# Performance work log

Measured on AMD Instinct MI355X. Metric: run time of the kernel, lower is better.

## Reference

```python
import jax, jax.numpy as jnp
import numpy as np

DN = ('NCHW', 'OIHW', 'NCHW')

def _conv(x, w, b, pad):
    y = jax.lax.conv_general_dilated(x, w, (1, 1), pad, dimension_numbers=DN)
    return y + b[None, :, None, None]

def setup_inputs() -> dict:
    key = jax.random.key(0)
    ks = jax.random.split(key, 8)
    B, C, H, W = 8, 256, 64, 64
    C8 = C // 8
    return {
        'x': jax.random.normal(ks[0], (B, C, H, W), jnp.float32),
        'wq': jax.random.normal(ks[1], (C8, C, 1, 3), jnp.float32) * 0.02,
        'bq': jax.random.normal(ks[2], (C8,), jnp.float32) * 0.02,
        'wk': jax.random.normal(ks[3], (C8, C, 3, 1), jnp.float32) * 0.02,
        'bk': jax.random.normal(ks[4], (C8,), jnp.float32) * 0.02,
        'wv': jax.random.normal(ks[5], (C, C, 1, 1), jnp.float32) * 0.02,
        'bv': jax.random.normal(ks[6], (C,), jnp.float32) * 0.02,
        'gamma': jax.random.normal(ks[7], (1,), jnp.float32),
    }

def reference(x, wq, bq, wk, bk, wv, bv, gamma):
    B, C, H, W = x.shape
    N = H * W
    # q: (1,3) kernel, pad (0,1); k: (3,1) kernel, pad (1,0); v: 1x1
    q = _conv(x, wq, bq, [(0, 0), (1, 1)]).reshape(B, -1, N)  # B, C/8, N
    k = _conv(x, wk, bk, [(1, 1), (0, 0)]).reshape(B, -1, N)  # B, C/8, N
    v = _conv(x, wv, bv, [(0, 0), (0, 0)]).reshape(B, C, N)   # B, C, N
    affinity = jnp.einsum('bci,bcj->bij', q, k)               # B, N, N
    affinity = jax.nn.softmax(affinity, axis=-1)
    # weights = v @ affinity^T  ->  (B, C, N)
    weights = jnp.einsum('bcj,bij->bci', v, affinity).reshape(B, C, H, W)
    return gamma[0] * weights + x
```

## Files before the change

kernel.cpp:

```cpp
#include <hip/hip_runtime.h>
#include <math.h>

#define BB 8
#define CCH 256
#define C8 32
#define NN 4096
#define LOG2E 1.44269504f

typedef unsigned short us;
typedef __attribute__((ext_vector_type(8))) short bf16x8;
typedef __attribute__((ext_vector_type(4))) float f32x4;
typedef __attribute__((ext_vector_type(16))) float f32x16;

static __device__ __forceinline__ us f2bf(float f) {
  union { float f; unsigned u; } v; v.f = f;
  unsigned r = v.u + 0x7fffu + ((v.u >> 16) & 1u);
  return (us)(r >> 16);
}

__global__ __launch_bounds__(256) void prep_kernel(
    const float* __restrict__ x, const float* __restrict__ wq,
    const float* __restrict__ wk, const float* __restrict__ wv,
    us* __restrict__ xT, us* __restrict__ wqc, us* __restrict__ wkc,
    us* __restrict__ wvb) {
  __shared__ __align__(16) us lt[64 * 68];
  int bid = blockIdx.x;
  int tid = threadIdx.x;
  if (bid < 2048) {
    int b = bid >> 8, cb = (bid >> 6) & 3, nb = bid & 63;
    const float* xb = x + (((size_t)(b * 256 + cb * 64)) << 12);
    int nl = tid & 63, ch = tid >> 6;
#pragma unroll
    for (int p = 0; p < 16; p++) {
      int c = p * 4 + ch;
      lt[nl * 68 + c] = f2bf(xb[((size_t)c << 12) + (nb * 64 + nl)]);
    }
    __syncthreads();
    us* xTb = xT + (((size_t)b << 12) + nb * 64) * 256 + cb * 64;
    int cw = tid & 7, nr0 = tid >> 3;
#pragma unroll
    for (int p2 = 0; p2 < 2; p2++) {
      int nr = p2 * 32 + nr0;
      uint2 lo = *(const uint2*)&lt[nr * 68 + cw * 8];
      uint2 hi = *(const uint2*)&lt[nr * 68 + cw * 8 + 4];
      *(uint4*)&xTb[(size_t)nr * 256 + cw * 8] = make_uint4(lo.x, lo.y, hi.x, hi.y);
    }
  } else {
    int idx = (bid - 2048) * 256 + tid;
    if (idx < 24576) {
      int oc = idx / 768, r = idx % 768, t = r >> 8, ic = r & 255;
      wqc[idx] = f2bf(wq[(oc * 256 + ic) * 3 + t] * LOG2E);
    } else if (idx < 49152) {
      int j = idx - 24576;
      int oc = j / 768, r = j % 768, t = r >> 8, ic = r & 255;
      wkc[j] = f2bf(wk[(oc * 256 + ic) * 3 + t]);
    } else if (idx < 114688) {
      int j = idx - 49152;
      wvb[j] = f2bf(wv[j]);
    }
  }
}

__global__ __launch_bounds__(256) void conv_kernel(
    const us* __restrict__ xT, const us* __restrict__ wqc,
    const us* __restrict__ wkc, const float* __restrict__ bq,
    const float* __restrict__ bk, const us* __restrict__ wvb,
    const float* __restrict__ bv, us* __restrict__ qT, us* __restrict__ kT,
    us* __restrict__ vblk) {
  int tid = threadIdx.x, lane = tid & 63, w = tid >> 6;
  int l15 = lane & 15, quad = lane >> 4;
  if (blockIdx.x < 512) {
    int bid = blockIdx.x;
    int b = bid & 7, rt = bid >> 3;
    int n0 = rt * 64, y = rt;
    bool isq = (w < 2);
    int m0 = (w & 1) * 16;
    const us* wc = isq ? wqc : wkc;
    const us* xTb = xT + (((size_t)b << 12) * 256);
    f32x4 acc[4];
#pragma unroll
    for (int nt = 0; nt < 4; nt++) acc[nt] = (f32x4){0.f, 0.f, 0.f, 0.f};
#pragma unroll
    for (int t = 0; t < 3; t++) {
      bool killT = (!isq) && ((t == 0 && y == 0) || (t == 2 && y == 63));
      if (!killT) {
        int dn = isq ? (t - 1) : (t - 1) * 64;
#pragma unroll
        for (int k8 = 0; k8 < 8; k8++) {
          int kloc = t * 256 + k8 * 32 + quad * 8;
          bf16x8 af = *(const bf16x8*)(wc + (size_t)(m0 + l15) * 768 + kloc);
          int ic = k8 * 32 + quad * 8;
#pragma unroll
          for (int nt = 0; nt < 4; nt++) {
            int nl = nt * 16 + l15;
            int ns = n0 + nl + dn;
            ns = ns < 0 ? 0 : (ns > 4095 ? 4095 : ns);
            bf16x8 bf = *(const bf16x8*)(xTb + (size_t)ns * 256 + ic);
            if (isq && ((t == 0 && nl == 0) || (t == 2 && nl == 63)))
              bf = (bf16x8){0, 0, 0, 0, 0, 0, 0, 0};
            acc[nt] = __builtin_amdgcn_mfma_f32_16x16x32_bf16(af, bf, acc[nt], 0, 0, 0);
          }
        }
      }
    }
    const float* bias = isq ? bq : bk;
    float bsc = isq ? LOG2E : 1.0f;
    us* outp = (isq ? qT : kT) + (((size_t)b << 12) * 32);
    float b0 = bias[m0 + quad * 4 + 0] * bsc;
    float b1 = bias[m0 + quad * 4 + 1] * bsc;
    float b2 = bias[m0 + quad * 4 + 2] * bsc;
    float b3 = bias[m0 + quad * 4 + 3] * bsc;
#pragma unroll
    for (int nt = 0; nt < 4; nt++) {
      int n = n0 + nt * 16 + l15;
      unsigned lo = (unsigned)f2bf(acc[nt][0] + b0) | ((unsigned)f2bf(acc[nt][1] + b1) << 16);
      unsigned hi = (unsigned)f2bf(acc[nt][2] + b2) | ((unsigned)f2bf(acc[nt][3] + b3) << 16);
      *(uint2*)(outp + (size_t)n * 32 + m0 + quad * 4) = make_uint2(lo, hi);
    }
  } else {
    int bid = blockIdx.x - 512;
    int b = bid & 7, nt0 = bid >> 3;
    int n0 = nt0 * 64;
    const us* xTb = xT + (((size_t)b << 12) * 256);
    f32x4 acc[4][4];
#pragma unroll
    for (int ct = 0; ct < 4; ct++)
#pragma unroll
      for (int nt = 0; nt < 4; nt++) acc[ct][nt] = (f32x4){0.f, 0.f, 0.f, 0.f};
#pragma unroll
    for (int kk = 0; kk < 8; kk++) {
      bf16x8 bfr[4];
#pragma unroll
      for (int nt = 0; nt < 4; nt++)
        bfr[nt] = *(const bf16x8*)(xTb + (size_t)(n0 + nt * 16 + l15) * 256 + kk * 32 + quad * 8);
#pragma unroll
      for (int ct = 0; ct < 4; ct++) {
        bf16x8 af = *(const bf16x8*)(wvb + (size_t)(w * 64 + ct * 16 + l15) * 256 + kk * 32 + quad * 8);
#pragma unroll
        for (int nt = 0; nt < 4; nt++)
          acc[ct][nt] = __builtin_amdgcn_mfma_f32_16x16x32_bf16(af, bfr[nt], acc[ct][nt], 0, 0, 0);
      }
    }
    us* vb = vblk + ((size_t)b << 20);
#pragma unroll
    for (int ct = 0; ct < 4; ct++) {
#pragma unroll
      for (int r = 0; r < 4; r++) {
        int oc = w * 64 + ct * 16 + quad * 4 + r;
        float bvv = bv[oc];
#pragma unroll
        for (int nt = 0; nt < 4; nt++) {
          vb[((size_t)((n0 >> 4) + nt) * 256 + oc) * 16 + l15] = f2bf(acc[ct][nt][r] + bvv);
        }
      }
    }
  }
}

__global__ __launch_bounds__(512, 4) void attn_kernel(
    const float* __restrict__ x, const us* __restrict__ qT,
    const us* __restrict__ kT, const us* __restrict__ vblk,
    const float* __restrict__ gamma_p, float* __restrict__ out) {
  __shared__ __align__(16) us pb[2][64 * 72];
  __shared__ float lpart[2][64];

  int tid = threadIdx.x, lane = tid & 63, w = tid >> 6;
  int l15 = lane & 15, quad = lane >> 4;
  int l31 = lane & 31, h32 = lane >> 5;
  int tw = w & 3, jh = w >> 2;

  int bid = blockIdx.x;
  int b = bid & 7, i0 = (bid >> 3) * 64;

  const us* qTb = qT + (((size_t)b << 12) * 32);
  const us* kTb = kT + (((size_t)b << 12) * 32);
  const us* vbb = vblk + ((size_t)b << 20);

  bf16x8 qf = *(const bf16x8*)(qTb + (size_t)(i0 + tw * 16 + l15) * 32 + quad * 8);

  const us* kbase = kTb + (size_t)(jh * 32 + l15) * 32 + quad * 8;
  const us* vbase = vbb + (size_t)(w * 32 + l31) * 16 + h32 * 8;
  int pwi = (tw * 16 + l15) * 72 + jh * 32 + quad * 4;
  int pri = l31 * 72 + h32 * 8;

  float lr = 0.f;
  f32x4 s0, s1;
  f32x16 o0, o1;
#pragma unroll
  for (int rg = 0; rg < 16; rg++) { o0[rg] = 0.f; o1[rg] = 0.f; }

  bf16x8 kS0a, kS0b, kS1a, kS1b;
  bf16x8 v0_0, v0_1, v0_2, v0_3;
  bf16x8 v1_0, v1_1, v1_2, v1_3;
  bf16x8 v2_0, v2_1, v2_2, v2_3;
  bf16x8 v3_0, v3_1, v3_2, v3_3;

#define PRE(JT, KN0, KN1, VN0, VN1, VN2, VN3)                                  \
  do {                                                                         \
    int jn = (JT) & 63;                                                        \
    const us* kp = kbase + (size_t)jn * 2048;                                  \
    const us* vp = vbase + (size_t)jn * 16384;                                 \
    KN0 = *(const bf16x8*)(kp);                                                \
    KN1 = *(const bf16x8*)(kp + 512);                                          \
    VN0 = *(const bf16x8*)(vp);                                                \
    VN1 = *(const bf16x8*)(vp + 4096);                                         \
    VN2 = *(const bf16x8*)(vp + 8192);                                         \
    VN3 = *(const bf16x8*)(vp + 12288);                                        \
  } while (0)

#define QKM(KC0, KC1)                                                          \
  do {                                                                         \
    s0 = __builtin_amdgcn_mfma_f32_16x16x32_bf16(KC0, qf, (f32x4){0.f, 0.f, 0.f, 0.f}, 0, 0, 0); \
    s1 = __builtin_amdgcn_mfma_f32_16x16x32_bf16(KC1, qf, (f32x4){0.f, 0.f, 0.f, 0.f}, 0, 0, 0); \
  } while (0)

#define PVM(BUFR, VP0, VP1, VP2, VP3)                                          \
  do {                                                                         \
    const us* pr = (const us*)pb + (BUFR) * (64 * 72) + pri;                   \
    __builtin_amdgcn_s_setprio(1);                                             \
    bf16x8 pf0, pf1;                                                           \
    pf0 = *(const bf16x8*)(pr + 0);                                            \
    pf1 = *(const bf16x8*)(pr + 32 * 72 + 0);                                  \
    o0 = __builtin_amdgcn_mfma_f32_32x32x16_bf16(VP0, pf0, o0, 0, 0, 0);       \
    o1 = __builtin_amdgcn_mfma_f32_32x32x16_bf16(VP0, pf1, o1, 0, 0, 0);       \
    pf0 = *(const bf16x8*)(pr + 16);                                           \
    pf1 = *(const bf16x8*)(pr + 32 * 72 + 16);                                 \
    o0 = __builtin_amdgcn_mfma_f32_32x32x16_bf16(VP1, pf0, o0, 0, 0, 0);       \
    o1 = __builtin_amdgcn_mfma_f32_32x32x16_bf16(VP1, pf1, o1, 0, 0, 0);       \
    pf0 = *(const bf16x8*)(pr + 32);                                           \
    pf1 = *(const bf16x8*)(pr + 32 * 72 + 32);                                 \
    o0 = __builtin_amdgcn_mfma_f32_32x32x16_bf16(VP2, pf0, o0, 0, 0, 0);       \
    o1 = __builtin_amdgcn_mfma_f32_32x32x16_bf16(VP2, pf1, o1, 0, 0, 0);       \
    pf0 = *(const bf16x8*)(pr + 48);                                           \
    pf1 = *(const bf16x8*)(pr + 32 * 72 + 48);                                 \
    o0 = __builtin_amdgcn_mfma_f32_32x32x16_bf16(VP3, pf0, o0, 0, 0, 0);       \
    o1 = __builtin_amdgcn_mfma_f32_32x32x16_bf16(VP3, pf1, o1, 0, 0, 0);       \
    __builtin_amdgcn_s_setprio(0);                                             \
  } while (0)

#define SMW(BUFW)                                                              \
  do {                                                                         \
    us* pw = (us*)pb + (BUFW) * (64 * 72) + pwi;                               \
    {                                                                          \
      float p0 = __builtin_amdgcn_exp2f(s0[0]);                                \
      float p1 = __builtin_amdgcn_exp2f(s0[1]);                                \
      float p2 = __builtin_amdgcn_exp2f(s0[2]);                                \
      float p3 = __builtin_amdgcn_exp2f(s0[3]);                                \
      lr += (p0 + p1) + (p2 + p3);                                             \
      unsigned e0, e1;                                                         \
      asm("v_cvt_pk_bf16_f32 %0, %1, %2" : "=v"(e0) : "v"(p0), "v"(p1));       \
      asm("v_cvt_pk_bf16_f32 %0, %1, %2" : "=v"(e1) : "v"(p2), "v"(p3));       \
      *(uint2*)pw = make_uint2(e0, e1);                                        \
    }                                                                          \
    {                                                                          \
      float p0 = __builtin_amdgcn_exp2f(s1[0]);                                \
      float p1 = __builtin_amdgcn_exp2f(s1[1]);                                \
      float p2 = __builtin_amdgcn_exp2f(s1[2]);                                \
      float p3 = __builtin_amdgcn_exp2f(s1[3]);                                \
      lr += (p0 + p1) + (p2 + p3);                                             \
      unsigned e0, e1;                                                         \
      asm("v_cvt_pk_bf16_f32 %0, %1, %2" : "=v"(e0) : "v"(p0), "v"(p1));       \
      asm("v_cvt_pk_bf16_f32 %0, %1, %2" : "=v"(e1) : "v"(p2), "v"(p3));       \
      *(uint2*)(pw + 16) = make_uint2(e0, e1);                                 \
    }                                                                          \
  } while (0)

#define BAR                                                                    \
  do {                                                                         \
    asm volatile("s_waitcnt lgkmcnt(0)" ::: "memory");                         \
    __builtin_amdgcn_s_barrier();                                              \
    __builtin_amdgcn_sched_barrier(0);                                         \
  } while (0)

  PRE(0, kS0a, kS0b, v0_0, v0_1, v0_2, v0_3);
  PRE(1, kS1a, kS1b, v1_0, v1_1, v1_2, v1_3);
  QKM(kS0a, kS0b);
  SMW(0);
  BAR;
  PRE(2, kS0a, kS0b, v2_0, v2_1, v2_2, v2_3);
  QKM(kS1a, kS1b);
  PVM(0, v0_0, v0_1, v0_2, v0_3);
  SMW(1);
  BAR;
  PRE(3, kS1a, kS1b, v3_0, v3_1, v3_2, v3_3);
  QKM(kS0a, kS0b);
  PVM(1, v1_0, v1_1, v1_2, v1_3);
  SMW(0);
  BAR;
  PRE(4, kS0a, kS0b, v0_0, v0_1, v0_2, v0_3);
  QKM(kS1a, kS1b);
  PVM(0, v2_0, v2_1, v2_2, v2_3);
  SMW(1);
  BAR;

  for (int n4 = 1; n4 < 16; n4++) {
    int n = n4 * 4;
    PRE(n + 1, kS1a, kS1b, v1_0, v1_1, v1_2, v1_3);
    QKM(kS0a, kS0b);
    PVM(1, v3_0, v3_1, v3_2, v3_3);
    SMW(0);
    BAR;
    PRE(n + 2, kS0a, kS0b, v2_0, v2_1, v2_2, v2_3);
    QKM(kS1a, kS1b);
    PVM(0, v0_0, v0_1, v0_2, v0_3);
    SMW(1);
    BAR;
    PRE(n + 3, kS1a, kS1b, v3_0, v3_1, v3_2, v3_3);
    QKM(kS0a, kS0b);
    PVM(1, v1_0, v1_1, v1_2, v1_3);
    SMW(0);
    BAR;
    PRE(n + 4, kS0a, kS0b, v0_0, v0_1, v0_2, v0_3);
    QKM(kS1a, kS1b);
    PVM(0, v2_0, v2_1, v2_2, v2_3);
    SMW(1);
    BAR;
  }
  PVM(1, v3_0, v3_1, v3_2, v3_3);

#undef PRE
#undef QKM
#undef PVM
#undef SMW
#undef BAR

  float lt = lr;
  lt += __shfl_xor(lt, 16);
  lt += __shfl_xor(lt, 32);
  if (quad == 0) lpart[jh][tw * 16 + l15] = lt;
  __syncthreads();
  float g = gamma_p[0];
  const float* xb = x + ((size_t)b << 20);
  float* ob = out + ((size_t)b << 20);
  float gl[2];
#pragma unroll
  for (int it = 0; it < 2; it++) {
    int i = it * 32 + l31;
    gl[it] = g / (lpart[0][i] + lpart[1][i]);
  }
#pragma unroll
  for (int it = 0; it < 2; it++) {
    int i = i0 + it * 32 + l31;
    const f32x16& o = (it == 0) ? o0 : o1;
#pragma unroll
    for (int rg = 0; rg < 16; rg++) {
      int c = w * 32 + ((rg & 3) + 8 * (rg >> 2) + 4 * h32);
      size_t idx = ((size_t)c << 12) + i;
      ob[idx] = o[rg] * gl[it] + xb[idx];
    }
  }
}

extern "C" void kernel_launch(void* const* d_in, const int* in_sizes, int n_in,
                              void* d_out, int out_size, void* d_ws, size_t ws_size,
                              hipStream_t stream) {
  const float* x = (const float*)d_in[0];
  const float* wq = (const float*)d_in[1];
  const float* bq = (const float*)d_in[2];
  const float* wk = (const float*)d_in[3];
  const float* bk = (const float*)d_in[4];
  const float* wv = (const float*)d_in[5];
  const float* bv = (const float*)d_in[6];
  const float* gamma = (const float*)d_in[7];
  float* out = (float*)d_out;

  us* xT = (us*)d_ws;
  us* qT = xT + (size_t)8388608;
  us* kT = qT + (size_t)1048576;
  us* vblk = kT + (size_t)1048576;
  us* wqc = vblk + (size_t)8388608;
  us* wkc = wqc + (size_t)24576;
  us* wvb = wkc + (size_t)24576;

  prep_kernel<<<2496, 256, 0, stream>>>(x, wq, wk, wv, xT, wqc, wkc, wvb);
  conv_kernel<<<1024, 256, 0, stream>>>(xT, wqc, wkc, bq, bk, wvb, bv, qT, kT, vblk);
  attn_kernel<<<512, 512, 0, stream>>>(x, qT, kT, vblk, gamma, out);
}
```

Baseline: 228.1 us.

## Fuse x transpose into conv kernel via swizzled LDS staging

Removes the separate prep pass that wrote a bf16 transposed copy of x to global memory. The conv kernel now loads a 256-row tile of x (with 64-row halos) directly from fp32, converts it to bf16 into an XOR-swizzled 128KB LDS buffer, and computes q, k and v projections from LDS. This cuts a global round trip and a launch, at the cost of large LDS use, 1024-thread blocks with one block per CU, and redundant halo loading.

```diff
diff --git a/kernel.cpp b/kernel.cpp
--- a/kernel.cpp
+++ b/kernel.cpp
@@ -1,10 +1,6 @@
 #include <hip/hip_runtime.h>
 #include <math.h>
 
-#define BB 8
-#define CCH 256
-#define C8 32
-#define NN 4096
 #define LOG2E 1.44269504f
 
 typedef unsigned short us;
@@ -18,87 +14,86 @@
   return (us)(r >> 16);
 }
 
-__global__ __launch_bounds__(256) void prep_kernel(
-    const float* __restrict__ x, const float* __restrict__ wq,
-    const float* __restrict__ wk, const float* __restrict__ wv,
-    us* __restrict__ xT, us* __restrict__ wqc, us* __restrict__ wkc,
+__global__ __launch_bounds__(256) void wrep_kernel(
+    const float* __restrict__ wq, const float* __restrict__ wk,
+    const float* __restrict__ wv, us* __restrict__ wqc, us* __restrict__ wkc,
     us* __restrict__ wvb) {
-  __shared__ __align__(16) us lt[64 * 68];
-  int bid = blockIdx.x;
-  int tid = threadIdx.x;
-  if (bid < 2048) {
-    int b = bid >> 8, cb = (bid >> 6) & 3, nb = bid & 63;
-    const float* xb = x + (((size_t)(b * 256 + cb * 64)) << 12);
-    int nl = tid & 63, ch = tid >> 6;
-#pragma unroll
-    for (int p = 0; p < 16; p++) {
-      int c = p * 4 + ch;
-      lt[nl * 68 + c] = f2bf(xb[((size_t)c << 12) + (nb * 64 + nl)]);
-    }
-    __syncthreads();
-    us* xTb = xT + (((size_t)b << 12) + nb * 64) * 256 + cb * 64;
-    int cw = tid & 7, nr0 = tid >> 3;
-#pragma unroll
-    for (int p2 = 0; p2 < 2; p2++) {
-      int nr = p2 * 32 + nr0;
-      uint2 lo = *(const uint2*)&lt[nr * 68 + cw * 8];
-      uint2 hi = *(const uint2*)&lt[nr * 68 + cw * 8 + 4];
-      *(uint4*)&xTb[(size_t)nr * 256 + cw * 8] = make_uint4(lo.x, lo.y, hi.x, hi.y);
-    }
-  } else {
-    int idx = (bid - 2048) * 256 + tid;
-    if (idx < 24576) {
-      int oc = idx / 768, r = idx % 768, t = r >> 8, ic = r & 255;
-      wqc[idx] = f2bf(wq[(oc * 256 + ic) * 3 + t] * LOG2E);
-    } else if (idx < 49152) {
-      int j = idx - 24576;
-      int oc = j / 768, r = j % 768, t = r >> 8, ic = r & 255;
-      wkc[j] = f2bf(wk[(oc * 256 + ic) * 3 + t]);
-    } else if (idx < 114688) {
-      int j = idx - 49152;
-      wvb[j] = f2bf(wv[j]);
-    }
-  }
-}
-
-__global__ __launch_bounds__(256) void conv_kernel(
-    const us* __restrict__ xT, const us* __restrict__ wqc,
+  int idx = blockIdx.x * 256 + threadIdx.x;
+  if (idx < 24576) {
+    int oc = idx / 768, r = idx % 768, t = r >> 8, ic = r & 255;
+    wqc[idx] = f2bf(wq[(oc * 256 + ic) * 3 + t] * LOG2E);
+  } else if (idx < 49152) {
+    int j = idx - 24576;
+    int oc = j / 768, r = j % 768, t = r >> 8, ic = r & 255;
+    wkc[j] = f2bf(wk[(oc * 256 + ic) * 3 + t]);
+  } else if (idx < 114688) {
+    int j = idx - 49152;
+    wvb[j] = f2bf(wv[j]);
+  }
+}
+
+__global__ __launch_bounds__(1024) void fconv_kernel(
+    const float* __restrict__ x, const us* __restrict__ wqc,
     const us* __restrict__ wkc, const float* __restrict__ bq,
     const float* __restrict__ bk, const us* __restrict__ wvb,
     const float* __restrict__ bv, us* __restrict__ qT, us* __restrict__ kT,
     us* __restrict__ vblk) {
+  __shared__ __align__(16) us xs[256 * 256];
+
   int tid = threadIdx.x, lane = tid & 63, w = tid >> 6;
   int l15 = lane & 15, quad = lane >> 4;
-  if (blockIdx.x < 512) {
-    int bid = blockIdx.x;
-    int b = bid & 7, rt = bid >> 3;
-    int n0 = rt * 64, y = rt;
-    bool isq = (w < 2);
-    int m0 = (w & 1) * 16;
+  int bid = blockIdx.x;
+  int b = bid >> 5, yt = bid & 31;
+  int no0 = yt * 128;
+  const float* xb = x + ((size_t)b << 20);
+
+#pragma unroll
+  for (int i = 0; i < 8; i++) {
+    int c0 = (w * 8 + i) * 2;
+    const float* xc0 = xb + ((size_t)c0 << 12);
+#pragma unroll
+    for (int rb = 0; rb < 4; rb++) {
+      int rr = rb * 64 + lane;
+      int gn = no0 - 64 + rr;
+      bool valid = (unsigned)gn < 4096u;
+      float a0 = valid ? xc0[gn] : 0.f;
+      float a1 = valid ? xc0[4096 + gn] : 0.f;
+      unsigned u;
+      asm("v_cvt_pk_bf16_f32 %0, %1, %2" : "=v"(u) : "v"(a0), "v"(a1));
+      int chunk = (c0 >> 3) ^ (rr & 31);
+      *(unsigned*)&xs[rr * 256 + chunk * 8 + (c0 & 7)] = u;
+    }
+  }
+  __syncthreads();
+
+  if (w < 8) {
+    bool isq = (w < 4);
+    int qw = isq ? w : (w - 4);
     const us* wc = isq ? wqc : wkc;
-    const us* xTb = xT + (((size_t)b << 12) * 256);
-    f32x4 acc[4];
-#pragma unroll
-    for (int nt = 0; nt < 4; nt++) acc[nt] = (f32x4){0.f, 0.f, 0.f, 0.f};
+    f32x4 acc00 = (f32x4){0.f, 0.f, 0.f, 0.f}, acc01 = acc00;
+    f32x4 acc10 = acc00, acc11 = acc00;
 #pragma unroll
     for (int t = 0; t < 3; t++) {
-      bool killT = (!isq) && ((t == 0 && y == 0) || (t == 2 && y == 63));
-      if (!killT) {
-        int dn = isq ? (t - 1) : (t - 1) * 64;
-#pragma unroll
-        for (int k8 = 0; k8 < 8; k8++) {
-          int kloc = t * 256 + k8 * 32 + quad * 8;
-          bf16x8 af = *(const bf16x8*)(wc + (size_t)(m0 + l15) * 768 + kloc);
-          int ic = k8 * 32 + quad * 8;
-#pragma unroll
-          for (int nt = 0; nt < 4; nt++) {
-            int nl = nt * 16 + l15;
-            int ns = n0 + nl + dn;
-            ns = ns < 0 ? 0 : (ns > 4095 ? 4095 : ns);
-            bf16x8 bf = *(const bf16x8*)(xTb + (size_t)ns * 256 + ic);
-            if (isq && ((t == 0 && nl == 0) || (t == 2 && nl == 63)))
-              bf = (bf16x8){0, 0, 0, 0, 0, 0, 0, 0};
-            acc[nt] = __builtin_amdgcn_mfma_f32_16x16x32_bf16(af, bf, acc[nt], 0, 0, 0);
+      int dn = isq ? (t - 1) : (t - 1) * 64;
+#pragma unroll
+      for (int k8 = 0; k8 < 8; k8++) {
+        int kloc = t * 256 + k8 * 32 + quad * 8;
+        bf16x8 af0 = *(const bf16x8*)(wc + (size_t)l15 * 768 + kloc);
+        bf16x8 af1 = *(const bf16x8*)(wc + (size_t)(16 + l15) * 768 + kloc);
+        int cb3 = (k8 * 32 + quad * 8) >> 3;
+#pragma unroll
+        for (int j = 0; j < 2; j++) {
+          int ntl = (qw * 2 + j) * 16 + l15;
+          int rr = 64 + ntl + dn;
+          bf16x8 bf = *(const bf16x8*)&xs[rr * 256 + ((cb3 ^ (rr & 31)) << 3)];
+          if (isq && ((t == 0 && (ntl & 63) == 0) || (t == 2 && (ntl & 63) == 63)))
+            bf = (bf16x8){0, 0, 0, 0, 0, 0, 0, 0};
+          if (j == 0) {
+            acc00 = __builtin_amdgcn_mfma_f32_16x16x32_bf16(af0, bf, acc00, 0, 0, 0);
+            acc10 = __builtin_amdgcn_mfma_f32_16x16x32_bf16(af1, bf, acc10, 0, 0, 0);
+          } else {
+            acc01 = __builtin_amdgcn_mfma_f32_16x16x32_bf16(af0, bf, acc01, 0, 0, 0);
+            acc11 = __builtin_amdgcn_mfma_f32_16x16x32_bf16(af1, bf, acc11, 0, 0, 0);
           }
         }
       }
@@ -106,52 +101,45 @@
     const float* bias = isq ? bq : bk;
     float bsc = isq ? LOG2E : 1.0f;
     us* outp = (isq ? qT : kT) + (((size_t)b << 12) * 32);
-    float b0 = bias[m0 + quad * 4 + 0] * bsc;
-    float b1 = bias[m0 + quad * 4 + 1] * bsc;
-    float b2 = bias[m0 + quad * 4 + 2] * bsc;
-    float b3 = bias[m0 + quad * 4 + 3] * bsc;
-#pragma unroll
-    for (int nt = 0; nt < 4; nt++) {
-      int n = n0 + nt * 16 + l15;
-      unsigned lo = (unsigned)f2bf(acc[nt][0] + b0) | ((unsigned)f2bf(acc[nt][1] + b1) << 16);
-      unsigned hi = (unsigned)f2bf(acc[nt][2] + b2) | ((unsigned)f2bf(acc[nt][3] + b3) << 16);
-      *(uint2*)(outp + (size_t)n * 32 + m0 + quad * 4) = make_uint2(lo, hi);
+#pragma unroll
+    for (int mo = 0; mo < 2; mo++) {
+      float b0 = bias[mo * 16 + quad * 4 + 0] * bsc;
+      float b1 = bias[mo * 16 + quad * 4 + 1] * bsc;
+      float b2 = bias[mo * 16 + quad * 4 + 2] * bsc;
+      float b3 = bias[mo * 16 + quad * 4 + 3] * bsc;
+#pragma unroll
+      for (int j = 0; j < 2; j++) {
+        f32x4 a = (mo == 0) ? (j == 0 ? acc00 : acc01) : (j == 0 ? acc10 : acc11);
+        int n = no0 + (qw * 2 + j) * 16 + l15;
+        unsigned lo = (unsigned)f2bf(a[0] + b0) | ((unsigned)f2bf(a[1] + b1) << 16);
+        unsigned hi = (unsigned)f2bf(a[2] + b2) | ((unsigned)f2bf(a[3] + b3) << 16);
+        *(uint2*)(outp + (size_t)n * 32 + mo * 16 + quad * 4) = make_uint2(lo, hi);
+      }
     }
   } else {
-    int bid = blockIdx.x - 512;
-    int b = bid & 7, nt0 = bid >> 3;
-    int n0 = nt0 * 64;
-    const us* xTb = xT + (((size_t)b << 12) * 256);
-    f32x4 acc[4][4];
-#pragma unroll
-    for (int ct = 0; ct < 4; ct++)
-#pragma unroll
-      for (int nt = 0; nt < 4; nt++) acc[ct][nt] = (f32x4){0.f, 0.f, 0.f, 0.f};
+    int nt = w - 8;
+    int rr = 64 + nt * 16 + l15;
+    f32x4 acc[16];
+#pragma unroll
+    for (int ot = 0; ot < 16; ot++) acc[ot] = (f32x4){0.f, 0.f, 0.f, 0.f};
 #pragma unroll
     for (int kk = 0; kk < 8; kk++) {
-      bf16x8 bfr[4];
-#pragma unroll
-      for (int nt = 0; nt < 4; nt++)
-        bfr[nt] = *(const bf16x8*)(xTb + (size_t)(n0 + nt * 16 + l15) * 256 + kk * 32 + quad * 8);
-#pragma unroll
-      for (int ct = 0; ct < 4; ct++) {
-        bf16x8 af = *(const bf16x8*)(wvb + (size_t)(w * 64 + ct * 16 + l15) * 256 + kk * 32 + quad * 8);
-#pragma unroll
-        for (int nt = 0; nt < 4; nt++)
-          acc[ct][nt] = __builtin_amdgcn_mfma_f32_16x16x32_bf16(af, bfr[nt], acc[ct][nt], 0, 0, 0);
+      int cb3 = (kk * 32 + quad * 8) >> 3;
+      bf16x8 bfr = *(const bf16x8*)&xs[rr * 256 + ((cb3 ^ (rr & 31)) << 3)];
+#pragma unroll
+      for (int ot = 0; ot < 16; ot++) {
+        bf16x8 af = *(const bf16x8*)(wvb + (size_t)(ot * 16 + l15) * 256 + kk * 32 + quad * 8);
+        acc[ot] = __builtin_amdgcn_mfma_f32_16x16x32_bf16(af, bfr, acc[ot], 0, 0, 0);
       }
     }
     us* vb = vblk + ((size_t)b << 20);
-#pragma unroll
-    for (int ct = 0; ct < 4; ct++) {
+    int n16 = yt * 8 + nt;
+#pragma unroll
+    for (int ot = 0; ot < 16; ot++) {
 #pragma unroll
       for (int r = 0; r < 4; r++) {
-        int oc = w * 64 + ct * 16 + quad * 4 + r;
-        float bvv = bv[oc];
-#pragma unroll
-        for (int nt = 0; nt < 4; nt++) {
-          vb[((size_t)((n0 >> 4) + nt) * 256 + oc) * 16 + l15] = f2bf(acc[ct][nt][r] + bvv);
-        }
+        int oc = ot * 16 + quad * 4 + r;
+        vb[((size_t)n16 * 256 + oc) * 16 + l15] = f2bf(acc[ot][r] + bv[oc]);
       }
     }
   }
@@ -364,15 +352,14 @@
   const float* gamma = (const float*)d_in[7];
   float* out = (float*)d_out;
 
-  us* xT = (us*)d_ws;
-  us* qT = xT + (size_t)8388608;
+  us* qT = (us*)d_ws;
   us* kT = qT + (size_t)1048576;
   us* vblk = kT + (size_t)1048576;
   us* wqc = vblk + (size_t)8388608;
   us* wkc = wqc + (size_t)24576;
   us* wvb = wkc + (size_t)24576;
 
-  prep_kernel<<<2496, 256, 0, stream>>>(x, wq, wk, wv, xT, wqc, wkc, wvb);
-  conv_kernel<<<1024, 256, 0, stream>>>(xT, wqc, wkc, bq, bk, wvb, bv, qT, kT, vblk);
+  wrep_kernel<<<448, 256, 0, stream>>>(wq, wk, wv, wqc, wkc, wvb);
+  fconv_kernel<<<256, 1024, 0, stream>>>(x, wqc, wkc, bq, bk, wvb, bv, qT, kT, vblk);
   attn_kernel<<<512, 512, 0, stream>>>(x, qT, kT, vblk, gamma, out);
 }
```

Result: slower. 239.2 us (+4.9%).

## Fuse prep, conv and attention into one cooperative persistent kernel

Applied to the files above, without the earlier changes.

Merges the three kernels into a single cooperative launch of 512 blocks of 512 threads. Grid-wide syncs separate the transpose/weight-cast, conv and attention phases, and a fallback path launches the same kernel three times with a phase mask. This removes two kernel launch gaps and tail drains, but the early phases now run on fewer, larger blocks, and the grid syncs add their own cost.

```diff
diff --git a/kernel.cpp b/kernel.cpp
--- a/kernel.cpp
+++ b/kernel.cpp
@@ -1,11 +1,10 @@
 #include <hip/hip_runtime.h>
+#include <hip/hip_cooperative_groups.h>
 #include <math.h>
 
-#define BB 8
-#define CCH 256
-#define C8 32
-#define NN 4096
 #define LOG2E 1.44269504f
+
+namespace cg = cooperative_groups;
 
 typedef unsigned short us;
 typedef __attribute__((ext_vector_type(8))) short bf16x8;
@@ -18,182 +17,175 @@
   return (us)(r >> 16);
 }
 
-__global__ __launch_bounds__(256) void prep_kernel(
+__global__ __launch_bounds__(512, 4) void mega_kernel(
     const float* __restrict__ x, const float* __restrict__ wq,
     const float* __restrict__ wk, const float* __restrict__ wv,
-    us* __restrict__ xT, us* __restrict__ wqc, us* __restrict__ wkc,
-    us* __restrict__ wvb) {
-  __shared__ __align__(16) us lt[64 * 68];
-  int bid = blockIdx.x;
-  int tid = threadIdx.x;
-  if (bid < 2048) {
-    int b = bid >> 8, cb = (bid >> 6) & 3, nb = bid & 63;
-    const float* xb = x + (((size_t)(b * 256 + cb * 64)) << 12);
-    int nl = tid & 63, ch = tid >> 6;
-#pragma unroll
-    for (int p = 0; p < 16; p++) {
-      int c = p * 4 + ch;
-      lt[nl * 68 + c] = f2bf(xb[((size_t)c << 12) + (nb * 64 + nl)]);
-    }
-    __syncthreads();
-    us* xTb = xT + (((size_t)b << 12) + nb * 64) * 256 + cb * 64;
-    int cw = tid & 7, nr0 = tid >> 3;
-#pragma unroll
-    for (int p2 = 0; p2 < 2; p2++) {
-      int nr = p2 * 32 + nr0;
-      uint2 lo = *(const uint2*)&lt[nr * 68 + cw * 8];
-      uint2 hi = *(const uint2*)&lt[nr * 68 + cw * 8 + 4];
-      *(uint4*)&xTb[(size_t)nr * 256 + cw * 8] = make_uint4(lo.x, lo.y, hi.x, hi.y);
-    }
-  } else {
-    int idx = (bid - 2048) * 256 + tid;
-    if (idx < 24576) {
-      int oc = idx / 768, r = idx % 768, t = r >> 8, ic = r & 255;
-      wqc[idx] = f2bf(wq[(oc * 256 + ic) * 3 + t] * LOG2E);
-    } else if (idx < 49152) {
-      int j = idx - 24576;
-      int oc = j / 768, r = j % 768, t = r >> 8, ic = r & 255;
-      wkc[j] = f2bf(wk[(oc * 256 + ic) * 3 + t]);
-    } else if (idx < 114688) {
-      int j = idx - 49152;
-      wvb[j] = f2bf(wv[j]);
-    }
-  }
-}
-
-__global__ __launch_bounds__(256) void conv_kernel(
-    const us* __restrict__ xT, const us* __restrict__ wqc,
-    const us* __restrict__ wkc, const float* __restrict__ bq,
-    const float* __restrict__ bk, const us* __restrict__ wvb,
-    const float* __restrict__ bv, us* __restrict__ qT, us* __restrict__ kT,
-    us* __restrict__ vblk) {
-  int tid = threadIdx.x, lane = tid & 63, w = tid >> 6;
-  int l15 = lane & 15, quad = lane >> 4;
-  if (blockIdx.x < 512) {
-    int bid = blockIdx.x;
-    int b = bid & 7, rt = bid >> 3;
-    int n0 = rt * 64, y = rt;
-    bool isq = (w < 2);
-    int m0 = (w & 1) * 16;
-    const us* wc = isq ? wqc : wkc;
-    const us* xTb = xT + (((size_t)b << 12) * 256);
-    f32x4 acc[4];
-#pragma unroll
-    for (int nt = 0; nt < 4; nt++) acc[nt] = (f32x4){0.f, 0.f, 0.f, 0.f};
-#pragma unroll
-    for (int t = 0; t < 3; t++) {
-      bool killT = (!isq) && ((t == 0 && y == 0) || (t == 2 && y == 63));
-      if (!killT) {
-        int dn = isq ? (t - 1) : (t - 1) * 64;
-#pragma unroll
-        for (int k8 = 0; k8 < 8; k8++) {
-          int kloc = t * 256 + k8 * 32 + quad * 8;
-          bf16x8 af = *(const bf16x8*)(wc + (size_t)(m0 + l15) * 768 + kloc);
-          int ic = k8 * 32 + quad * 8;
-#pragma unroll
-          for (int nt = 0; nt < 4; nt++) {
-            int nl = nt * 16 + l15;
-            int ns = n0 + nl + dn;
-            ns = ns < 0 ? 0 : (ns > 4095 ? 4095 : ns);
-            bf16x8 bf = *(const bf16x8*)(xTb + (size_t)ns * 256 + ic);
-            if (isq && ((t == 0 && nl == 0) || (t == 2 && nl == 63)))
-              bf = (bf16x8){0, 0, 0, 0, 0, 0, 0, 0};
-            acc[nt] = __builtin_amdgcn_mfma_f32_16x16x32_bf16(af, bf, acc[nt], 0, 0, 0);
-          }
-        }
-      }
-    }
-    const float* bias = isq ? bq : bk;
-    float bsc = isq ? LOG2E : 1.0f;
-    us* outp = (isq ? qT : kT) + (((size_t)b << 12) * 32);
-    float b0 = bias[m0 + quad * 4 + 0] * bsc;
-    float b1 = bias[m0 + quad * 4 + 1] * bsc;
-    float b2 = bias[m0 + quad * 4 + 2] * bsc;
-    float b3 = bias[m0 + quad * 4 + 3] * bsc;
-#pragma unroll
-    for (int nt = 0; nt < 4; nt++) {
-      int n = n0 + nt * 16 + l15;
-      unsigned lo = (unsigned)f2bf(acc[nt][0] + b0) | ((unsigned)f2bf(acc[nt][1] + b1) << 16);
-      unsigned hi = (unsigned)f2bf(acc[nt][2] + b2) | ((unsigned)f2bf(acc[nt][3] + b3) << 16);
-      *(uint2*)(outp + (size_t)n * 32 + m0 + quad * 4) = make_uint2(lo, hi);
-    }
-  } else {
-    int bid = blockIdx.x - 512;
-    int b = bid & 7, nt0 = bid >> 3;
-    int n0 = nt0 * 64;
-    const us* xTb = xT + (((size_t)b << 12) * 256);
-    f32x4 acc[4][4];
-#pragma unroll
-    for (int ct = 0; ct < 4; ct++)
-#pragma unroll
-      for (int nt = 0; nt < 4; nt++) acc[ct][nt] = (f32x4){0.f, 0.f, 0.f, 0.f};
-#pragma unroll
-    for (int kk = 0; kk < 8; kk++) {
-      bf16x8 bfr[4];
-#pragma unroll
-      for (int nt = 0; nt < 4; nt++)
-        bfr[nt] = *(const bf16x8*)(xTb + (size_t)(n0 + nt * 16 + l15) * 256 + kk * 32 + quad * 8);
-#pragma unroll
-      for (int ct = 0; ct < 4; ct++) {
-        bf16x8 af = *(const bf16x8*)(wvb + (size_t)(w * 64 + ct * 16 + l15) * 256 + kk * 32 + quad * 8);
-#pragma unroll
-        for (int nt = 0; nt < 4; nt++)
-          acc[ct][nt] = __builtin_amdgcn_mfma_f32_16x16x32_bf16(af, bfr[nt], acc[ct][nt], 0, 0, 0);
-      }
-    }
-    us* vb = vblk + ((size_t)b << 20);
-#pragma unroll
-    for (int ct = 0; ct < 4; ct++) {
-#pragma unroll
-      for (int r = 0; r < 4; r++) {
-        int oc = w * 64 + ct * 16 + quad * 4 + r;
-        float bvv = bv[oc];
-#pragma unroll
-        for (int nt = 0; nt < 4; nt++) {
-          vb[((size_t)((n0 >> 4) + nt) * 256 + oc) * 16 + l15] = f2bf(acc[ct][nt][r] + bvv);
-        }
-      }
-    }
-  }
-}
-
-__global__ __launch_bounds__(512, 4) void attn_kernel(
-    const float* __restrict__ x, const us* __restrict__ qT,
-    const us* __restrict__ kT, const us* __restrict__ vblk,
-    const float* __restrict__ gamma_p, float* __restrict__ out) {
-  __shared__ __align__(16) us pb[2][64 * 72];
-  __shared__ float lpart[2][64];
+    const float* __restrict__ bq, const float* __restrict__ bk,
+    const float* __restrict__ bv, const float* __restrict__ gamma_p,
+    float* __restrict__ out, us* __restrict__ xT, us* __restrict__ qT,
+    us* __restrict__ kT, us* __restrict__ vblk, us* __restrict__ wqc,
+    us* __restrict__ wkc, us* __restrict__ wvb, int pm) {
+  __shared__ __align__(16) union {
+    us lt[64 * 68];
+    struct {
+      us pb[2][64 * 72];
+      float lpart[2][64];
+    } c;
+  } sm;
 
   int tid = threadIdx.x, lane = tid & 63, w = tid >> 6;
   int l15 = lane & 15, quad = lane >> 4;
   int l31 = lane & 31, h32 = lane >> 5;
-  int tw = w & 3, jh = w >> 2;
-
   int bid = blockIdx.x;
-  int b = bid & 7, i0 = (bid >> 3) * 64;
-
-  const us* qTb = qT + (((size_t)b << 12) * 32);
-  const us* kTb = kT + (((size_t)b << 12) * 32);
-  const us* vbb = vblk + ((size_t)b << 20);
-
-  bf16x8 qf = *(const bf16x8*)(qTb + (size_t)(i0 + tw * 16 + l15) * 32 + quad * 8);
-
-  const us* kbase = kTb + (size_t)(jh * 32 + l15) * 32 + quad * 8;
-  const us* vbase = vbb + (size_t)(w * 32 + l31) * 16 + h32 * 8;
-  int pwi = (tw * 16 + l15) * 72 + jh * 32 + quad * 4;
-  int pri = l31 * 72 + h32 * 8;
-
-  float lr = 0.f;
-  f32x4 s0, s1;
-  f32x16 o0, o1;
-#pragma unroll
-  for (int rg = 0; rg < 16; rg++) { o0[rg] = 0.f; o1[rg] = 0.f; }
-
-  bf16x8 kS0a, kS0b, kS1a, kS1b;
-  bf16x8 v0_0, v0_1, v0_2, v0_3;
-  bf16x8 v1_0, v1_1, v1_2, v1_3;
-  bf16x8 v2_0, v2_1, v2_2, v2_3;
-  bf16x8 v3_0, v3_1, v3_2, v3_3;
+  int b = bid & 7, u = bid >> 3;
+
+  if (pm & 1) {
+    int nb = u;
+    int nl = tid & 63, ch = tid >> 6;
+#pragma unroll 1
+    for (int cb = 0; cb < 4; cb++) {
+      const float* xb = x + (((size_t)(b * 256 + cb * 64)) << 12);
+#pragma unroll
+      for (int p = 0; p < 8; p++) {
+        int c = p * 8 + ch;
+        sm.lt[nl * 68 + c] = f2bf(xb[((size_t)c << 12) + (nb * 64 + nl)]);
+      }
+      __syncthreads();
+      us* xTb = xT + (((size_t)b << 12) + nb * 64) * 256 + cb * 64;
+      int cw = tid & 7, nr = tid >> 3;
+      uint2 lo = *(const uint2*)&sm.lt[nr * 68 + cw * 8];
+      uint2 hi = *(const uint2*)&sm.lt[nr * 68 + cw * 8 + 4];
+      *(uint4*)&xTb[(size_t)nr * 256 + cw * 8] = make_uint4(lo.x, lo.y, hi.x, hi.y);
+      __syncthreads();
+    }
+    if (tid < 224) {
+      int idx = bid * 224 + tid;
+      if (idx < 24576) {
+        int oc = idx / 768, r = idx % 768, t = r >> 8, ic = r & 255;
+        wqc[idx] = f2bf(wq[(oc * 256 + ic) * 3 + t] * LOG2E);
+      } else if (idx < 49152) {
+        int j = idx - 24576;
+        int oc = j / 768, r = j % 768, t = r >> 8, ic = r & 255;
+        wkc[j] = f2bf(wk[(oc * 256 + ic) * 3 + t]);
+      } else {
+        int j = idx - 49152;
+        wvb[j] = f2bf(wv[j]);
+      }
+    }
+  }
+  if (pm == 7) cg::this_grid().sync();
+
+  if (pm & 2) {
+    const us* xTb = xT + (((size_t)b << 12) * 256);
+    int n0 = u * 64, y = u;
+    if (w < 4) {
+      bool isq = (w < 2);
+      int m0 = (w & 1) * 16;
+      const us* wc = isq ? wqc : wkc;
+      f32x4 acc[4];
+#pragma unroll
+      for (int nt = 0; nt < 4; nt++) acc[nt] = (f32x4){0.f, 0.f, 0.f, 0.f};
+#pragma unroll
+      for (int t = 0; t < 3; t++) {
+        bool killT = (!isq) && ((t == 0 && y == 0) || (t == 2 && y == 63));
+        if (!killT) {
+          int dn = isq ? (t - 1) : (t - 1) * 64;
+#pragma unroll
+          for (int k8 = 0; k8 < 8; k8++) {
+            int kloc = t * 256 + k8 * 32 + quad * 8;
+            bf16x8 af = *(const bf16x8*)(wc + (size_t)(m0 + l15) * 768 + kloc);
+            int ic = k8 * 32 + quad * 8;
+#pragma unroll
+            for (int nt = 0; nt < 4; nt++) {
+              int nl = nt * 16 + l15;
+              int ns = n0 + nl + dn;
+              ns = ns < 0 ? 0 : (ns > 4095 ? 4095 : ns);
+              bf16x8 bf = *(const bf16x8*)(xTb + (size_t)ns * 256 + ic);
+              if (isq && ((t == 0 && nl == 0) || (t == 2 && nl == 63)))
+                bf = (bf16x8){0, 0, 0, 0, 0, 0, 0, 0};
+              acc[nt] = __builtin_amdgcn_mfma_f32_16x16x32_bf16(af, bf, acc[nt], 0, 0, 0);
+            }
+          }
+        }
+      }
+      const float* bias = isq ? bq : bk;
+      float bsc = isq ? LOG2E : 1.0f;
+      us* outp = (isq ? qT : kT) + (((size_t)b << 12) * 32);
+      float b0 = bias[m0 + quad * 4 + 0] * bsc;
+      float b1 = bias[m0 + quad * 4 + 1] * bsc;
+      float b2 = bias[m0 + quad * 4 + 2] * bsc;
+      float b3 = bias[m0 + quad * 4 + 3] * bsc;
+#pragma unroll
+      for (int nt = 0; nt < 4; nt++) {
+        int n = n0 + nt * 16 + l15;
+        unsigned lo = (unsigned)f2bf(acc[nt][0] + b0) | ((unsigned)f2bf(acc[nt][1] + b1) << 16);
+        unsigned hi = (unsigned)f2bf(acc[nt][2] + b2) | ((unsigned)f2bf(acc[nt][3] + b3) << 16);
+        *(uint2*)(outp + (size_t)n * 32 + m0 + quad * 4) = make_uint2(lo, hi);
+      }
+    } else {
+      int wv4 = w - 4;
+      f32x4 acc[4][4];
+#pragma unroll
+      for (int ct = 0; ct < 4; ct++)
+#pragma unroll
+        for (int nt = 0; nt < 4; nt++) acc[ct][nt] = (f32x4){0.f, 0.f, 0.f, 0.f};
+#pragma unroll
+      for (int kk = 0; kk < 8; kk++) {
+        bf16x8 bfr[4];
+#pragma unroll
+        for (int nt = 0; nt < 4; nt++)
+          bfr[nt] = *(const bf16x8*)(xTb + (size_t)(n0 + nt * 16 + l15) * 256 + kk * 32 + quad * 8);
+#pragma unroll
+        for (int ct = 0; ct < 4; ct++) {
+          bf16x8 af = *(const bf16x8*)(wvb + (size_t)(wv4 * 64 + ct * 16 + l15) * 256 + kk * 32 + quad * 8);
+#pragma unroll
+          for (int nt = 0; nt < 4; nt++)
+            acc[ct][nt] = __builtin_amdgcn_mfma_f32_16x16x32_bf16(af, bfr[nt], acc[ct][nt], 0, 0, 0);
+        }
+      }
+      us* vb = vblk + ((size_t)b << 20);
+#pragma unroll
+      for (int ct = 0; ct < 4; ct++) {
+#pragma unroll
+        for (int r = 0; r < 4; r++) {
+          int oc = wv4 * 64 + ct * 16 + quad * 4 + r;
+          float bvv = bv[oc];
+#pragma unroll
+          for (int nt = 0; nt < 4; nt++) {
+            vb[((size_t)(u * 4 + nt) * 256 + oc) * 16 + l15] = f2bf(acc[ct][nt][r] + bvv);
+          }
+        }
+      }
+    }
+  }
+  if (pm == 7) cg::this_grid().sync();
+
+  if (pm & 4) {
+    int tw = w & 3, jh = w >> 2;
+    int i0 = u * 64;
+
+    const us* qTb = qT + (((size_t)b << 12) * 32);
+    const us* kTb = kT + (((size_t)b << 12) * 32);
+    const us* vbb = vblk + ((size_t)b << 20);
+
+    bf16x8 qf = *(const bf16x8*)(qTb + (size_t)(i0 + tw * 16 + l15) * 32 + quad * 8);
+
+    const us* kbase = kTb + (size_t)(jh * 32 + l15) * 32 + quad * 8;
+    const us* vbase = vbb + (size_t)(w * 32 + l31) * 16 + h32 * 8;
+    int pwi = (tw * 16 + l15) * 72 + jh * 32 + quad * 4;
+    int pri = l31 * 72 + h32 * 8;
+
+    float lr = 0.f;
+    f32x4 s0, s1;
+    f32x16 o0, o1;
+#pragma unroll
+    for (int rg = 0; rg < 16; rg++) { o0[rg] = 0.f; o1[rg] = 0.f; }
+
+    bf16x8 kS0a, kS0b, kS1a, kS1b;
+    bf16x8 v0_0, v0_1, v0_2, v0_3;
+    bf16x8 v1_0, v1_1, v1_2, v1_3;
+    bf16x8 v2_0, v2_1, v2_2, v2_3;
+    bf16x8 v3_0, v3_1, v3_2, v3_3;
 
 #define PRE(JT, KN0, KN1, VN0, VN1, VN2, VN3)                                  \
   do {                                                                         \
@@ -216,7 +208,7 @@
 
 #define PVM(BUFR, VP0, VP1, VP2, VP3)                                          \
   do {                                                                         \
-    const us* pr = (const us*)pb + (BUFR) * (64 * 72) + pri;                   \
+    const us* pr = (const us*)sm.c.pb + (BUFR) * (64 * 72) + pri;              \
     __builtin_amdgcn_s_setprio(1);                                             \
     bf16x8 pf0, pf1;                                                           \
     pf0 = *(const bf16x8*)(pr + 0);                                            \
@@ -240,7 +232,7 @@
 
 #define SMW(BUFW)                                                              \
   do {                                                                         \
-    us* pw = (us*)pb + (BUFW) * (64 * 72) + pwi;                               \
+    us* pw = (us*)sm.c.pb + (BUFW) * (64 * 72) + pwi;                          \
     {                                                                          \
       float p0 = __builtin_amdgcn_exp2f(s0[0]);                                \
       float p1 = __builtin_amdgcn_exp2f(s0[1]);                                \
@@ -272,51 +264,51 @@
     __builtin_amdgcn_sched_barrier(0);                                         \
   } while (0)
 
-  PRE(0, kS0a, kS0b, v0_0, v0_1, v0_2, v0_3);
-  PRE(1, kS1a, kS1b, v1_0, v1_1, v1_2, v1_3);
-  QKM(kS0a, kS0b);
-  SMW(0);
-  BAR;
-  PRE(2, kS0a, kS0b, v2_0, v2_1, v2_2, v2_3);
-  QKM(kS1a, kS1b);
-  PVM(0, v0_0, v0_1, v0_2, v0_3);
-  SMW(1);
-  BAR;
-  PRE(3, kS1a, kS1b, v3_0, v3_1, v3_2, v3_3);
-  QKM(kS0a, kS0b);
-  PVM(1, v1_0, v1_1, v1_2, v1_3);
-  SMW(0);
-  BAR;
-  PRE(4, kS0a, kS0b, v0_0, v0_1, v0_2, v0_3);
-  QKM(kS1a, kS1b);
-  PVM(0, v2_0, v2_1, v2_2, v2_3);
-  SMW(1);
-  BAR;
-
-  for (int n4 = 1; n4 < 16; n4++) {
-    int n = n4 * 4;
-    PRE(n + 1, kS1a, kS1b, v1_0, v1_1, v1_2, v1_3);
+    PRE(0, kS0a, kS0b, v0_0, v0_1, v0_2, v0_3);
+    PRE(1, kS1a, kS1b, v1_0, v1_1, v1_2, v1_3);
     QKM(kS0a, kS0b);
-    PVM(1, v3_0, v3_1, v3_2, v3_3);
     SMW(0);
     BAR;
-    PRE(n + 2, kS0a, kS0b, v2_0, v2_1, v2_2, v2_3);
+    PRE(2, kS0a, kS0b, v2_0, v2_1, v2_2, v2_3);
     QKM(kS1a, kS1b);
     PVM(0, v0_0, v0_1, v0_2, v0_3);
     SMW(1);
     BAR;
-    PRE(n + 3, kS1a, kS1b, v3_0, v3_1, v3_2, v3_3);
+    PRE(3, kS1a, kS1b, v3_0, v3_1, v3_2, v3_3);
     QKM(kS0a, kS0b);
     PVM(1, v1_0, v1_1, v1_2, v1_3);
     SMW(0);
     BAR;
-    PRE(n + 4, kS0a, kS0b, v0_0, v0_1, v0_2, v0_3);
+    PRE(4, kS0a, kS0b, v0_0, v0_1, v0_2, v0_3);
     QKM(kS1a, kS1b);
     PVM(0, v2_0, v2_1, v2_2, v2_3);
     SMW(1);
     BAR;
-  }
-  PVM(1, v3_0, v3_1, v3_2, v3_3);
+
+    for (int n4 = 1; n4 < 16; n4++) {
+      int n = n4 * 4;
+      PRE(n + 1, kS1a, kS1b, v1_0, v1_1, v1_2, v1_3);
+      QKM(kS0a, kS0b);
+      PVM(1, v3_0, v3_1, v3_2, v3_3);
+      SMW(0);
+      BAR;
+      PRE(n + 2, kS0a, kS0b, v2_0, v2_1, v2_2, v2_3);
+      QKM(kS1a, kS1b);
+      PVM(0, v0_0, v0_1, v0_2, v0_3);
+      SMW(1);
+      BAR;
+      PRE(n + 3, kS1a, kS1b, v3_0, v3_1, v3_2, v3_3);
+      QKM(kS0a, kS0b);
+      PVM(1, v1_0, v1_1, v1_2, v1_3);
+      SMW(0);
+      BAR;
+      PRE(n + 4, kS0a, kS0b, v0_0, v0_1, v0_2, v0_3);
+      QKM(kS1a, kS1b);
+      PVM(0, v2_0, v2_1, v2_2, v2_3);
+      SMW(1);
+      BAR;
+    }
+    PVM(1, v3_0, v3_1, v3_2, v3_3);
 
 #undef PRE
 #undef QKM
@@ -324,29 +316,30 @@
 #undef SMW
 #undef BAR
 
-  float lt = lr;
-  lt += __shfl_xor(lt, 16);
-  lt += __shfl_xor(lt, 32);
-  if (quad == 0) lpart[jh][tw * 16 + l15] = lt;
-  __syncthreads();
-  float g = gamma_p[0];
-  const float* xb = x + ((size_t)b << 20);
-  float* ob = out + ((size_t)b << 20);
-  float gl[2];
-#pragma unroll
-  for (int it = 0; it < 2; it++) {
-    int i = it * 32 + l31;
-    gl[it] = g / (lpart[0][i] + lpart[1][i]);
-  }
-#pragma unroll
-  for (int it = 0; it < 2; it++) {
-    int i = i0 + it * 32 + l31;
-    const f32x16& o = (it == 0) ? o0 : o1;
-#pragma unroll
-    for (int rg = 0; rg < 16; rg++) {
-      int c = w * 32 + ((rg & 3) + 8 * (rg >> 2) + 4 * h32);
-      size_t idx = ((size_t)c << 12) + i;
-      ob[idx] = o[rg] * gl[it] + xb[idx];
+    float lt2 = lr;
+    lt2 += __shfl_xor(lt2, 16);
+    lt2 += __shfl_xor(lt2, 32);
+    if (quad == 0) sm.c.lpart[jh][tw * 16 + l15] = lt2;
+    __syncthreads();
+    float g = gamma_p[0];
+    const float* xb = x + ((size_t)b << 20);
+    float* ob = out + ((size_t)b << 20);
+    float gl[2];
+#pragma unroll
+    for (int it = 0; it < 2; it++) {
+      int i = it * 32 + l31;
+      gl[it] = g / (sm.c.lpart[0][i] + sm.c.lpart[1][i]);
+    }
+#pragma unroll
+    for (int it = 0; it < 2; it++) {
+      int i = i0 + it * 32 + l31;
+      const f32x16& o = (it == 0) ? o0 : o1;
+#pragma unroll
+      for (int rg = 0; rg < 16; rg++) {
+        int c = w * 32 + ((rg & 3) + 8 * (rg >> 2) + 4 * h32);
+        size_t idx = ((size_t)c << 12) + i;
+        ob[idx] = o[rg] * gl[it] + xb[idx];
+      }
     }
   }
 }
@@ -372,7 +365,20 @@
   us* wkc = wqc + (size_t)24576;
   us* wvb = wkc + (size_t)24576;
 
-  prep_kernel<<<2496, 256, 0, stream>>>(x, wq, wk, wv, xT, wqc, wkc, wvb);
-  conv_kernel<<<1024, 256, 0, stream>>>(xT, wqc, wkc, bq, bk, wvb, bv, qT, kT, vblk);
-  attn_kernel<<<512, 512, 0, stream>>>(x, qT, kT, vblk, gamma, out);
+  int pm_all = 7;
+  void* args[] = {(void*)&x,    (void*)&wq,   (void*)&wk,   (void*)&wv,
+                  (void*)&bq,   (void*)&bk,   (void*)&bv,   (void*)&gamma,
+                  (void*)&out,  (void*)&xT,   (void*)&qT,   (void*)&kT,
+                  (void*)&vblk, (void*)&wqc,  (void*)&wkc,  (void*)&wvb,
+                  (void*)&pm_all};
+  hipError_t e = hipLaunchCooperativeKernel((const void*)mega_kernel, dim3(512),
+                                            dim3(512), args, 0, stream);
+  if (e != hipSuccess) {
+    mega_kernel<<<512, 512, 0, stream>>>(x, wq, wk, wv, bq, bk, bv, gamma, out,
+                                         xT, qT, kT, vblk, wqc, wkc, wvb, 1);
+    mega_kernel<<<512, 512, 0, stream>>>(x, wq, wk, wv, bq, bk, bv, gamma, out,
+                                         xT, qT, kT, vblk, wqc, wkc, wvb, 2);
+    mega_kernel<<<512, 512, 0, stream>>>(x, wq, wk, wv, bq, bk, bv, gamma, out,
+                                         xT, qT, kT, vblk, wqc, wkc, wvb, 4);
+  }
 }
```

Result: slower. 384.4 us (+68.5%).
